# Kernel optimization log

Hardware: AMD Instinct MI355X
Metric: run time of the kernel (lower is better)

## Reference

```python
import jax, jax.numpy as jnp
import numpy as np

N_POS = 10  # number of child positions encoded in U_f (10*h_size rows)


def setup_inputs() -> dict:
    key = jax.random.key(0)
    ks = jax.random.split(key, 12)
    N, H = 32768, 128
    s = 0.05  # keep activations in a sane range
    return {
        "child_h": jax.random.normal(ks[0], (N, 1, H), jnp.float32),
        "child_c": jax.random.normal(ks[1], (N, 1, H), jnp.float32),
        "extra_input_depth_1": jax.random.normal(ks[2], (N, H), jnp.float32),
        "extra_input_depth_2": jax.random.normal(ks[3], (N, H), jnp.float32),
        "h_prev": jax.random.normal(ks[4], (N, H), jnp.float32),
        "pos": jax.random.randint(ks[5], (N,), 0, N_POS, jnp.int32),
        "depth": jax.random.randint(ks[6], (N,), 0, 4, jnp.int32),
        "mask": jax.random.randint(ks[7], (N,), 0, 2, jnp.int32),
        "W_f": jax.random.normal(ks[8], (N_POS * H, H), jnp.float32) * s,
        "b_f": jax.random.normal(ks[9], (N_POS * H,), jnp.float32) * s,
        "W_iou": jax.random.normal(ks[10], (3 * H, N_POS * H), jnp.float32) * s,
        "b_iou": jax.random.normal(ks[11], (1, 3 * H), jnp.float32) * s,
    }


def reference(child_h, child_c, extra_input_depth_1, extra_input_depth_2,
              h_prev, pos, depth, mask, W_f, b_f, W_iou, b_iou):
    N, _, H = child_h.shape
    dt = child_h.dtype
    # reduce_func: flatten mailbox (single child => last_dim == h_size)
    h_cat = child_h.reshape(N, H)
    # masked injection of extra inputs by depth
    h_cat = h_cat + extra_input_depth_2 * (depth == 2).astype(dt)[:, None]
    h_cat = h_cat + extra_input_depth_1 * (depth == 1).astype(dt)[:, None]
    # per-position grouped matmuls against weight slices, scattered back by pos mask
    W_f_r = W_f.reshape(N_POS, H, H)          # row slice pos*H:(pos+1)*H
    b_f_r = b_f.reshape(N_POS, H)
    W_iou_r = W_iou.reshape(3 * H, N_POS, H)  # col slice pos*H:(pos+1)*H
    u = jnp.zeros((N, H), dt)
    iou = jnp.zeros((N, 3 * H), dt)
    for p in range(N_POS):  # small fixed group count
        sel = (pos == p)[:, None]
        u = jnp.where(sel, h_cat @ W_f_r[p] + b_f_r[p][None, :], u)
        iou = jnp.where(sel, h_cat @ W_iou_r[:, p, :].T, iou)
    # sigmoid forget gate, children-sum of cell states
    f = jax.nn.sigmoid(u)
    c_red = jnp.sum(f[:, None, :] * child_c, axis=1)  # [N, H]
    # apply_node_func
    iou = iou + b_iou
    i, o, uu = jnp.split(iou, 3, axis=1)
    c_new = jax.nn.sigmoid(i) * jnp.tanh(uu) + c_red
    h_new = jax.nn.sigmoid(o) * jnp.tanh(c_new)
    # update_masked_nodes=False: blend (note: DGL node 'c' was overwritten by reduce)
    m = mask.astype(dt)[:, None]
    h = h_prev * m + (1.0 - m) * h_new
    c = c_red * m + (1.0 - m) * c_new
    return h, c
```

## Files before the change

kernel.cpp:

```cpp
#include <hip/hip_runtime.h>

#define H 128
#define NPOS 10
#define ROWSB 32
#define BLOCK 512
#define NXCD 8

using bf16x8 = __attribute__((ext_vector_type(8))) short;
using f32x4  = __attribute__((ext_vector_type(4))) float;

__device__ __forceinline__ unsigned short f2bf(float f) {
  unsigned u = __float_as_uint(f);
  u += 0x7FFFu + ((u >> 16) & 1u);
  return (unsigned short)(u >> 16);
}
__device__ __forceinline__ float bf2f(unsigned short s) {
  return __uint_as_float(((unsigned)s) << 16);
}
__device__ __forceinline__ float sigm(float x) {
  return __builtin_amdgcn_rcpf(1.0f + __builtin_amdgcn_exp2f(-1.44269504f * x));
}
__device__ __forceinline__ float tanh_f(float x) {
  return 2.0f * __builtin_amdgcn_rcpf(1.0f + __builtin_amdgcn_exp2f(-2.88539008f * x)) - 1.0f;
}

__global__ void prep_wt(const float* __restrict__ Wf, const float* __restrict__ Wiou,
                        unsigned short* __restrict__ wt,
                        const int* __restrict__ posp, int* __restrict__ hist2,
                        int N, int nhb) {
  int b = blockIdx.x, t = threadIdx.x;
  if (b < NPOS * 16) {
    __shared__ float tile[32][33];
    int p = b >> 4, jt = (b >> 2) & 3, kt = b & 3;
    int tx = t & 31, ty = t >> 5;
    #pragma unroll
    for (int it = 0; it < 4; ++it) {
      int krow = kt * 32 + ty + it * 8;
      int j = jt * 32 + tx;
      tile[ty + it * 8][tx] = Wf[(size_t)(p * H + krow) * H + j];
    }
    __syncthreads();
    #pragma unroll
    for (int it = 0; it < 4; ++it) {
      int j2 = jt * 32 + ty + it * 8;
      size_t dst = (((size_t)(p * 4 + kt) * 4 + (tx >> 3)) * 512 + j2) * 8 + (tx & 7);
      wt[dst] = f2bf(tile[tx][ty + it * 8]);
    }
  } else if (b < NPOS * 16 + (NPOS * 384 * H) / 256) {
    int id = (b - NPOS * 16) * 256 + t;
    int p = id / 49152;
    int r = id - p * 49152;
    int j = 128 + (r >> 7);
    int k = r & 127;
    float v = Wiou[(size_t)(r >> 7) * (NPOS * H) + p * H + k];
    size_t dst = (((size_t)(p * 4 + (k >> 5)) * 4 + ((k >> 3) & 3)) * 512 + j) * 8 + (k & 7);
    wt[dst] = f2bf(v);
  } else {
    int hb = b - (NPOS * 16 + (NPOS * 384 * H) / 256);
    __shared__ int c[NPOS];
    if (t < NPOS) c[t] = 0;
    __syncthreads();
    int i = hb * 256 + t;
    if (i < N) atomicAdd(&c[posp[i]], 1);
    __syncthreads();
    if (t < NPOS) hist2[hb * 16 + t] = c[t];
  }
}

__global__ void scan_build(const int* __restrict__ hist2, int nhb,
                           int* __restrict__ off2,
                           int* __restrict__ blkpos, int* __restrict__ blkgs,
                           int* __restrict__ blkcnt, int maxb) {
  __shared__ int tot[NPOS], base[NPOS + 1], bb[NPOS + 1];
  int t = threadIdx.x;
  int w = t >> 6, l = t & 63;
  if (w < NPOS) {
    int b0 = 2 * l, b1 = 2 * l + 1;
    int a  = (b0 < nhb) ? hist2[b0 * 16 + w] : 0;
    int bv = (b1 < nhb) ? hist2[b1 * 16 + w] : 0;
    int s = a + bv, sc = s;
    #pragma unroll
    for (int off = 1; off < 64; off <<= 1) {
      int u = __shfl_up(sc, off);
      if (l >= off) sc += u;
    }
    int excl = sc - s;
    if (b0 < nhb) off2[b0 * 16 + w] = excl;
    if (b1 < nhb) off2[b1 * 16 + w] = excl + a;
    if (l == 63) tot[w] = sc;
  }
  __syncthreads();
  if (t == 0) {
    int run = 0, rb = 0;
    for (int p = 0; p < NPOS; ++p) {
      base[p] = run; bb[p] = rb;
      run += tot[p];
      rb += (tot[p] + ROWSB - 1) / ROWSB;
    }
    base[NPOS] = run; bb[NPOS] = rb;
  }
  __syncthreads();
  for (int i = t; i < nhb * NPOS; i += 640) {
    int b = i / NPOS, p = i - b * NPOS;
    off2[b * 16 + p] += base[p];
  }
  int nb = bb[NPOS];
  for (int b = t; b < maxb; b += 640) {
    if (b < nb) {
      int p = 0;
      while (bb[p + 1] <= b) ++p;
      int s = (b - bb[p]) * ROWSB;
      blkpos[b] = p;
      blkgs[b] = base[p] + s;
      blkcnt[b] = min(ROWSB, tot[p] - s);
    } else {
      blkpos[b] = -1;
    }
  }
}

__global__ void scatter_idx(const int* __restrict__ posp, const int* __restrict__ depthp,
                            const int* __restrict__ maskp, const int* __restrict__ off2,
                            unsigned* __restrict__ order, int N) {
  __shared__ int c[NPOS], basearr[NPOS];
  int hb = blockIdx.x, t = threadIdx.x;
  if (t < NPOS) { c[t] = 0; basearr[t] = off2[hb * 16 + t]; }
  __syncthreads();
  int i = hb * 256 + t;
  int p = -1, r = 0;
  unsigned e = 0;
  if (i < N) {
    p = posp[i];
    r = atomicAdd(&c[p], 1);
    int d = depthp[i];
    int mk = maskp[i];
    e = (unsigned)i | ((unsigned)mk << 16) |
        ((unsigned)(d == 1) << 17) | ((unsigned)(d == 2) << 18);
  }
  __syncthreads();
  if (p >= 0) order[basearr[p] + r] = e;
}

__global__ __launch_bounds__(BLOCK, 3) void tree_lstm_main(
    const float* __restrict__ child_h, const float* __restrict__ child_c,
    const float* __restrict__ e1, const float* __restrict__ e2,
    const float* __restrict__ h_prev,
    const float* __restrict__ b_f, const float* __restrict__ b_iou,
    const unsigned short* __restrict__ wt,
    const unsigned* __restrict__ order, const int* __restrict__ blkpos,
    const int* __restrict__ blkgs, const int* __restrict__ blkcnt,
    float* __restrict__ out, int N, int nwg) {

  int orig = blockIdx.x;
  int q = nwg / NXCD, rres = nwg % NXCD;
  int xcd = orig % NXCD, slot = orig / NXCD;
  int b = (xcd < rres ? xcd * (q + 1) : rres * (q + 1) + (xcd - rres) * q) + slot;

  const int p = blkpos[b];
  if (p < 0) return;
  const int gs = blkgs[b], cnth = blkcnt[b];

  __shared__ unsigned short hs[ROWSB * H];
  __shared__ unsigned short Bs[4 * 512 * 8];
  __shared__ unsigned rowg[ROWSB];

  const int t = threadIdx.x;
  const int wv = t >> 6, l = t & 63;
  const int l15 = l & 15, lhi = l >> 4;
  const int colr = wv * 16 + l15;

  if (t < ROWSB) rowg[t] = (t < cnth) ? order[gs + t] : 0xFFFFFFFFu;
  __syncthreads();

  {
    int row = t >> 4, c8 = t & 15;
    unsigned e = rowg[row];
    float4 a0 = {0.f, 0.f, 0.f, 0.f}, a1 = {0.f, 0.f, 0.f, 0.f};
    if ((int)e >= 0) {
      int g = e & 0xFFFF;
      const float4* ph = (const float4*)(child_h + (size_t)g * H + c8 * 8);
      a0 = ph[0]; a1 = ph[1];
      if (e & (3u << 17)) {
        const float* ep = (e & (1u << 17)) ? e1 : e2;
        const float4* pe = (const float4*)(ep + (size_t)g * H + c8 * 8);
        float4 b0 = pe[0], b1 = pe[1];
        a0.x += b0.x; a0.y += b0.y; a0.z += b0.z; a0.w += b0.w;
        a1.x += b1.x; a1.y += b1.y; a1.z += b1.z; a1.w += b1.w;
      }
    }
    bf16x8 v;
    v[0] = (short)f2bf(a0.x); v[1] = (short)f2bf(a0.y);
    v[2] = (short)f2bf(a0.z); v[3] = (short)f2bf(a0.w);
    v[4] = (short)f2bf(a1.x); v[5] = (short)f2bf(a1.y);
    v[6] = (short)f2bf(a1.z); v[7] = (short)f2bf(a1.w);
    int wb = (row * 256 + c8 * 16) ^ ((row & 7) << 4);
    *(bf16x8*)((char*)hs + wb) = v;
  }
  __syncthreads();

  f32x4 acc[2][4] = {};
  const unsigned short* wtp = wt + (size_t)p * 65536;

  #pragma unroll
  for (int kk = 0; kk < 4; ++kk) {
    if (kk) __syncthreads();
    #pragma unroll
    for (int i = 0; i < 4; ++i) {
      int eo = (i * BLOCK + t) * 8;
      *(bf16x8*)(Bs + eo) = *(const bf16x8*)(wtp + kk * 16384 + eo);
    }
    __syncthreads();

    bf16x8 bfr[4];
    #pragma unroll
    for (int g4 = 0; g4 < 4; ++g4)
      bfr[g4] = *(const bf16x8*)(Bs + ((lhi * 512) + (g4 * 128 + colr)) * 8);

    #pragma unroll
    for (int c = 0; c < 2; ++c) {
      const int arow = c * 16 + l15;
      int rb = (arow * 256 + kk * 64 + lhi * 16) ^ ((arow & 7) << 4);
      bf16x8 afr = *(const bf16x8*)((const char*)hs + rb);
      #pragma unroll
      for (int g4 = 0; g4 < 4; ++g4)
        acc[c][g4] = __builtin_amdgcn_mfma_f32_16x16x32_bf16(afr, bfr[g4], acc[c][g4], 0, 0, 0);
    }
  }
  __syncthreads();

  {
    const float bfv = b_f[p * H + colr];
    const float b_i = b_iou[colr], b_o = b_iou[H + colr], b_g = b_iou[2 * H + colr];
    #pragma unroll
    for (int c = 0; c < 2; ++c)
      #pragma unroll
      for (int q = 0; q < 4; ++q) {
        int r = c * 16 + lhi * 4 + q;
        #pragma unroll
        for (int g4 = 0; g4 < 4; ++g4) {
          int rg = r * 4 + g4;
          int col = colr ^ (((rg >> 2) & 3) << 3);
          float v = (g4 == 0) ? acc[c][0][q] + bfv :
                    (g4 == 1) ? acc[c][1][q] + b_i :
                    (g4 == 2) ? acc[c][2][q] + b_o : acc[c][3][q] + b_g;
          Bs[(rg << 7) + col] = f2bf(v);
        }
      }
  }
  __syncthreads();

  const size_t NH = (size_t)N * H;
  const int c2 = 2 * l;
  #pragma unroll
  for (int j = 0; j < 4; ++j) {
    int r = wv * 4 + j;
    unsigned e = rowg[r];
    if ((int)e >= 0) {
      int g = e & 0xFFFF;
      int mi = (e >> 16) & 1;
      int rg0 = r * 4;
      unsigned uw = *(const unsigned*)&Bs[((rg0 + 0) << 7) + (c2 ^ ((((rg0 + 0) >> 2) & 3) << 3))];
      unsigned iw = *(const unsigned*)&Bs[((rg0 + 1) << 7) + (c2 ^ ((((rg0 + 1) >> 2) & 3) << 3))];
      unsigned ow = *(const unsigned*)&Bs[((rg0 + 2) << 7) + (c2 ^ ((((rg0 + 2) >> 2) & 3) << 3))];
      unsigned gw = *(const unsigned*)&Bs[((rg0 + 3) << 7) + (c2 ^ ((((rg0 + 3) >> 2) & 3) << 3))];
      float2 ccv = *(const float2*)(child_c + (size_t)g * H + c2);
      float f0 = sigm(bf2f((unsigned short)(uw & 0xFFFF)));
      float f1 = sigm(bf2f((unsigned short)(uw >> 16)));
      float cr0 = f0 * ccv.x, cr1 = f1 * ccv.y;
      float h0, h1, cv0, cv1;
      if (mi) {
        float2 hp = *(const float2*)(h_prev + (size_t)g * H + c2);
        h0 = hp.x; h1 = hp.y; cv0 = cr0; cv1 = cr1;
      } else {
        float i0 = sigm(bf2f((unsigned short)(iw & 0xFFFF)));
        float i1 = sigm(bf2f((unsigned short)(iw >> 16)));
        float g0 = tanh_f(bf2f((unsigned short)(gw & 0xFFFF)));
        float g1 = tanh_f(bf2f((unsigned short)(gw >> 16)));
        float o0 = sigm(bf2f((unsigned short)(ow & 0xFFFF)));
        float o1 = sigm(bf2f((unsigned short)(ow >> 16)));
        cv0 = i0 * g0 + cr0;
        cv1 = i1 * g1 + cr1;
        h0 = o0 * tanh_f(cv0);
        h1 = o1 * tanh_f(cv1);
      }
      size_t gi = (size_t)g * H + c2;
      __builtin_nontemporal_store(h0, &out[gi]);
      __builtin_nontemporal_store(h1, &out[gi + 1]);
      __builtin_nontemporal_store(cv0, &out[NH + gi]);
      __builtin_nontemporal_store(cv1, &out[NH + gi + 1]);
    }
  }
}

extern "C" void kernel_launch(void* const* d_in, const int* in_sizes, int n_in,
                              void* d_out, int out_size, void* d_ws, size_t ws_size,
                              hipStream_t stream) {
  const float* child_h = (const float*)d_in[0];
  const float* child_c = (const float*)d_in[1];
  const float* e1      = (const float*)d_in[2];
  const float* e2      = (const float*)d_in[3];
  const float* h_prev  = (const float*)d_in[4];
  const int*   posp    = (const int*)d_in[5];
  const int*   depthp  = (const int*)d_in[6];
  const int*   maskp   = (const int*)d_in[7];
  const float* W_f     = (const float*)d_in[8];
  const float* b_f     = (const float*)d_in[9];
  const float* W_iou   = (const float*)d_in[10];
  const float* b_iou   = (const float*)d_in[11];
  float* out = (float*)d_out;
  int N = in_sizes[0] / H;
  int nhb = (N + 255) / 256;
  int maxb = NPOS + N / ROWSB;

  unsigned short* wt = (unsigned short*)d_ws;
  int* hist2  = (int*)((char*)d_ws + (size_t)NPOS * 512 * H * 2);
  int* off2   = hist2 + nhb * 16;
  int* blkpos = off2 + nhb * 16;
  int* blkgs  = blkpos + maxb;
  int* blkcnt = blkgs + maxb;
  unsigned* order = (unsigned*)(blkcnt + maxb);

  int prep_blocks = NPOS * 16 + (NPOS * 384 * H) / 256 + nhb;
  hipLaunchKernelGGL(prep_wt, dim3(prep_blocks), dim3(256), 0, stream,
                     W_f, W_iou, wt, posp, hist2, N, nhb);
  hipLaunchKernelGGL(scan_build, dim3(1), dim3(640), 0, stream,
                     hist2, nhb, off2, blkpos, blkgs, blkcnt, maxb);
  hipLaunchKernelGGL(scatter_idx, dim3(nhb), dim3(256), 0, stream,
                     posp, depthp, maskp, off2, order, N);
  hipLaunchKernelGGL(tree_lstm_main, dim3(maxb), dim3(BLOCK), 0, stream,
                     child_h, child_c, e1, e2, h_prev,
                     b_f, b_iou, wt, order, blkpos, blkgs, blkcnt, out, N, maxb);
}
```

Measured before the change: 43.63 us.

## Bucket rows by (window, pos) to keep gathered rows spatially local

Changes the counting sort so rows are grouped by position within windows of 8 histogram blocks (2048 rows), rather than globally by position. Each main-kernel block then reads child/extra/h_prev rows from a narrow index range, which should improve cache and DRAM locality of the gather. The cost is more partially filled 32-row blocks, since each (window, pos) bucket rounds up separately, and a serial scan over 160 buckets in the single-block scan kernel.

Result: slower. 61.50 us (+41.0%).

```diff
diff --git a/kernel.cpp b/kernel.cpp
--- a/kernel.cpp
+++ b/kernel.cpp
@@ -5,6 +5,7 @@
 #define ROWSB 32
 #define BLOCK 512
 #define NXCD 8
+#define WINHB 8
 
 using bf16x8 = __attribute__((ext_vector_type(8))) short;
 using f32x4  = __attribute__((ext_vector_type(4))) float;
@@ -70,51 +71,48 @@
 __global__ void scan_build(const int* __restrict__ hist2, int nhb,
                            int* __restrict__ off2,
                            int* __restrict__ blkpos, int* __restrict__ blkgs,
-                           int* __restrict__ blkcnt, int maxb) {
-  __shared__ int tot[NPOS], base[NPOS + 1], bb[NPOS + 1];
+                           int* __restrict__ blkcnt, int maxb, int nwin) {
+  __shared__ int tot[176], base[177], bb[177];
   int t = threadIdx.x;
-  int w = t >> 6, l = t & 63;
-  if (w < NPOS) {
-    int b0 = 2 * l, b1 = 2 * l + 1;
-    int a  = (b0 < nhb) ? hist2[b0 * 16 + w] : 0;
-    int bv = (b1 < nhb) ? hist2[b1 * 16 + w] : 0;
-    int s = a + bv, sc = s;
-    #pragma unroll
-    for (int off = 1; off < 64; off <<= 1) {
-      int u = __shfl_up(sc, off);
-      if (l >= off) sc += u;
-    }
-    int excl = sc - s;
-    if (b0 < nhb) off2[b0 * 16 + w] = excl;
-    if (b1 < nhb) off2[b1 * 16 + w] = excl + a;
-    if (l == 63) tot[w] = sc;
+  int nbk = nwin * NPOS;
+  if (t < nbk) {
+    int w = t / NPOS, p = t - w * NPOS;
+    int hb1 = min((w + 1) * WINHB, nhb);
+    int run = 0;
+    for (int hb = w * WINHB; hb < hb1; ++hb) {
+      off2[hb * 16 + p] = run;
+      run += hist2[hb * 16 + p];
+    }
+    tot[t] = run;
   }
   __syncthreads();
   if (t == 0) {
     int run = 0, rb = 0;
-    for (int p = 0; p < NPOS; ++p) {
-      base[p] = run; bb[p] = rb;
-      run += tot[p];
-      rb += (tot[p] + ROWSB - 1) / ROWSB;
-    }
-    base[NPOS] = run; bb[NPOS] = rb;
-  }
-  __syncthreads();
-  for (int i = t; i < nhb * NPOS; i += 640) {
-    int b = i / NPOS, p = i - b * NPOS;
-    off2[b * 16 + p] += base[p];
-  }
-  int nb = bb[NPOS];
-  for (int b = t; b < maxb; b += 640) {
-    if (b < nb) {
-      int p = 0;
-      while (bb[p + 1] <= b) ++p;
-      int s = (b - bb[p]) * ROWSB;
-      blkpos[b] = p;
-      blkgs[b] = base[p] + s;
-      blkcnt[b] = min(ROWSB, tot[p] - s);
+    for (int bk = 0; bk < nbk; ++bk) {
+      base[bk] = run; bb[bk] = rb;
+      run += tot[bk];
+      rb += (tot[bk] + ROWSB - 1) / ROWSB;
+    }
+    base[nbk] = run; bb[nbk] = rb;
+  }
+  __syncthreads();
+  if (t < nbk) {
+    int w = t / NPOS, p = t - w * NPOS;
+    int hb1 = min((w + 1) * WINHB, nhb);
+    for (int hb = w * WINHB; hb < hb1; ++hb)
+      off2[hb * 16 + p] += base[t];
+  }
+  int nb = bb[nbk];
+  for (int b2 = t; b2 < maxb; b2 += 640) {
+    if (b2 < nb) {
+      int bk = 0;
+      while (bb[bk + 1] <= b2) ++bk;
+      int s = (b2 - bb[bk]) * ROWSB;
+      blkpos[b2] = bk % NPOS;
+      blkgs[b2] = base[bk] + s;
+      blkcnt[b2] = min(ROWSB, tot[bk] - s);
     } else {
-      blkpos[b] = -1;
+      blkpos[b2] = -1;
     }
   }
 }
@@ -234,15 +232,15 @@
     #pragma unroll
     for (int c = 0; c < 2; ++c)
       #pragma unroll
-      for (int q = 0; q < 4; ++q) {
-        int r = c * 16 + lhi * 4 + q;
+      for (int q2 = 0; q2 < 4; ++q2) {
+        int r = c * 16 + lhi * 4 + q2;
         #pragma unroll
         for (int g4 = 0; g4 < 4; ++g4) {
           int rg = r * 4 + g4;
           int col = colr ^ (((rg >> 2) & 3) << 3);
-          float v = (g4 == 0) ? acc[c][0][q] + bfv :
-                    (g4 == 1) ? acc[c][1][q] + b_i :
-                    (g4 == 2) ? acc[c][2][q] + b_o : acc[c][3][q] + b_g;
+          float v = (g4 == 0) ? acc[c][0][q2] + bfv :
+                    (g4 == 1) ? acc[c][1][q2] + b_i :
+                    (g4 == 2) ? acc[c][2][q2] + b_o : acc[c][3][q2] + b_g;
           Bs[(rg << 7) + col] = f2bf(v);
         }
       }
@@ -310,7 +308,8 @@
   float* out = (float*)d_out;
   int N = in_sizes[0] / H;
   int nhb = (N + 255) / 256;
-  int maxb = NPOS + N / ROWSB;
+  int nwin = (nhb + WINHB - 1) / WINHB;
+  int maxb = nwin * NPOS + N / ROWSB;
 
   unsigned short* wt = (unsigned short*)d_ws;
   int* hist2  = (int*)((char*)d_ws + (size_t)NPOS * 512 * H * 2);
@@ -324,7 +323,7 @@
   hipLaunchKernelGGL(prep_wt, dim3(prep_blocks), dim3(256), 0, stream,
                      W_f, W_iou, wt, posp, hist2, N, nhb);
   hipLaunchKernelGGL(scan_build, dim3(1), dim3(640), 0, stream,
-                     hist2, nhb, off2, blkpos, blkgs, blkcnt, maxb);
+                     hist2, nhb, off2, blkpos, blkgs, blkcnt, maxb, nwin);
   hipLaunchKernelGGL(scatter_idx, dim3(nhb), dim3(256), 0, stream,
                      posp, depthp, maskp, off2, order, N);
   hipLaunchKernelGGL(tree_lstm_main, dim3(maxb), dim3(BLOCK), 0, stream,
```
